# Kernel tuning notes

Measured on AMD Instinct MI355X. Metric: run time of the kernel, lower is better.

The kernel has to match this reference:

```python
import jax, jax.numpy as jnp
import numpy as np

B, S, E, H = 2, 2048, 1024, 16
D = E // H  # head_dim = 64


def setup_inputs() -> dict:
    key = jax.random.key(0)
    ks = jax.random.split(key, 8)
    s = 0.02
    return {
        "queries": jax.random.normal(ks[0], (B, S, E), jnp.float32),
        "keys": jax.random.normal(ks[1], (B, S, E), jnp.float32),
        "values": jax.random.normal(ks[2], (B, S, E), jnp.float32),
        "mask": jnp.ones((B, 1, 1, S), jnp.int32),
        "Wq": jax.random.normal(ks[3], (E, E), jnp.float32) * s,
        "bq": jnp.zeros((E,), jnp.float32),
        "Wk": jax.random.normal(ks[4], (E, E), jnp.float32) * s,
        "bk": jnp.zeros((E,), jnp.float32),
        "Wv": jax.random.normal(ks[5], (E, E), jnp.float32) * s,
        "bv": jnp.zeros((E,), jnp.float32),
        "Wo": jax.random.normal(ks[6], (E, E), jnp.float32) * s,
        "bo": jnp.zeros((E,), jnp.float32),
    }


def reference(queries, keys, values, mask, Wq, bq, Wk, bk, Wv, bv, Wo, bo):
    # NOTE: faithful to source, W_v is applied to the `keys` input; `values` is unused.
    q = queries @ Wq.T + bq            # [B,S,E]
    k = keys @ Wk.T + bk               # [B,S,E]
    v = keys @ Wv.T + bv               # [B,S,E]
    q = q.reshape(B, S, H, D)
    k = k.reshape(B, S, H, D)
    v = v.reshape(B, S, H, D)
    scale = 1.0 / jnp.sqrt(jnp.asarray(D, q.dtype))
    scores = jnp.einsum("nqhd,nkhd->nhqk", q, k)   # [B,H,S,S] full score matrix
    scores = jnp.where(mask == 0, jnp.asarray(-1e20, scores.dtype), scores)
    attn = jax.nn.softmax(scores * scale, axis=-1)
    out = jnp.einsum("nhqk,nkhd->nqhd", attn, v).reshape(B, S, E)
    return out @ Wo.T + bo
```

## Files before the change

kernel.cpp:

```cpp
#include <hip/hip_runtime.h>
#include <hip/hip_bf16.h>
#include <stdint.h>

#define NB 2
#define NS 2048
#define NE 1024
#define NH 16
#define ND 64
#define NT 32

typedef __attribute__((ext_vector_type(4))) float f32x4;
typedef __attribute__((ext_vector_type(16))) float f32x16;
typedef __attribute__((ext_vector_type(8))) short s16x8;
typedef __attribute__((ext_vector_type(4))) unsigned short u16x4;
typedef __attribute__((ext_vector_type(2))) unsigned int uint2v;

__device__ __forceinline__ unsigned short f2bf(float f) {
  union { float f; unsigned int i; } u; u.f = f;
  unsigned int r = u.i + 0x7FFFu + ((u.i >> 16) & 1u);
  return (unsigned short)(r >> 16);
}

__device__ __forceinline__ unsigned cvtpk_bf16(float lo, float hi) {
  unsigned r;
  asm("v_cvt_pk_bf16_f32 %0, %1, %2" : "=v"(r) : "v"(lo), "v"(hi));
  return r;
}

__device__ __forceinline__ void gload_lds16(const void* g, void* l) {
  __builtin_amdgcn_global_load_lds(
      (const __attribute__((address_space(1))) uint32_t*)g,
      (__attribute__((address_space(3))) uint32_t*)l, 16, 0, 0);
}

__device__ __forceinline__ f32x4 mfma16(s16x8 a, s16x8 b, f32x4 c) {
  return __builtin_amdgcn_mfma_f32_16x16x32_bf16(a, b, c, 0, 0, 0);
}
__device__ __forceinline__ f32x16 mfma32(s16x8 a, s16x8 b, f32x16 c) {
  return __builtin_amdgcn_mfma_f32_32x32x16_bf16(a, b, c, 0, 0, 0);
}

__global__ void conv_x2(const float* __restrict__ a, const float* __restrict__ b,
                        unsigned short* __restrict__ da, unsigned short* __restrict__ db,
                        int n4) {
  const float* s = blockIdx.y ? b : a;
  unsigned short* d = blockIdx.y ? db : da;
  int i = blockIdx.x * blockDim.x + threadIdx.x;
  int stride = gridDim.x * blockDim.x;
  for (; i < n4; i += stride) {
    float4 v = ((const float4*)s)[i];
    u16x4 o;
    o.x = f2bf(v.x); o.y = f2bf(v.y); o.z = f2bf(v.z); o.w = f2bf(v.w);
    ((u16x4*)d)[i] = o;
  }
}

__global__ void conv_w4(const float* __restrict__ s0, const float* __restrict__ s1,
                        const float* __restrict__ s2, const float* __restrict__ s3,
                        unsigned short* __restrict__ d0, unsigned short* __restrict__ d1,
                        unsigned short* __restrict__ d2, unsigned short* __restrict__ d3,
                        int n4) {
  const float* s; unsigned short* d;
  switch (blockIdx.y) {
    case 0: s = s0; d = d0; break;
    case 1: s = s1; d = d1; break;
    case 2: s = s2; d = d2; break;
    default: s = s3; d = d3; break;
  }
  int i = blockIdx.x * blockDim.x + threadIdx.x;
  int stride = gridDim.x * blockDim.x;
  for (; i < n4; i += stride) {
    float4 v = ((const float4*)s)[i];
    u16x4 o;
    o.x = f2bf(v.x); o.y = f2bf(v.y); o.z = f2bf(v.z); o.w = f2bf(v.w);
    ((u16x4*)d)[i] = o;
  }
}

__global__ void mask_pack(const int* __restrict__ mask, unsigned long long* __restrict__ bm) {
  int w = blockIdx.x;
  int lane = threadIdx.x;
  int mk = mask[w * 64 + lane];
  unsigned long long bal = __ballot(mk != 0);
  if (lane == 0) bm[w] = bal;
}

__global__ __launch_bounds__(256, 3) void gemm_qkv(
    const unsigned short* __restrict__ Aq, const unsigned short* __restrict__ Akv,
    const unsigned short* __restrict__ Wqp, const unsigned short* __restrict__ Wkp,
    const unsigned short* __restrict__ Wvp,
    const float* __restrict__ bqp, const float* __restrict__ bkp, const float* __restrict__ bvp,
    unsigned short* __restrict__ outq, unsigned short* __restrict__ outk,
    unsigned short* __restrict__ outvt) {
  constexpr int BM = 64, K = 1024;
  __shared__ char smem[2 * (BM * 128 + 16384)];
  const int t = threadIdx.x;
  const int lane = t & 63;
  const int wv = t >> 6;
  const int wr = wv >> 1, wc = wv & 1;
  const int x = blockIdx.x;
  const int bm = blockIdx.y * BM;
  const int lr = lane & 15, lg = lane >> 4;

  const unsigned short* A; const unsigned short* Wp; const float* bp;
  unsigned short* outp; int nloc, mode;
  float qsc;
  if (x < 8)       { A = Aq;  Wp = Wqp; bp = bqp; outp = outq;  nloc = x * 128;        mode = 0; qsc = 0.18033688f; }
  else if (x < 16) { A = Akv; Wp = Wkp; bp = bkp; outp = outk;  nloc = (x - 8) * 128;  mode = 0; qsc = 1.0f; }
  else             { A = Akv; Wp = Wvp; bp = bvp; outp = outvt; nloc = (x - 16) * 128; mode = 1; qsc = 1.0f; }

  f32x4 acc[2][4] = {};

  auto stage = [&](int buf, int k0) {
    char* As = smem + buf * (BM * 128 + 16384);
    char* Bs = As + BM * 128;
#pragma unroll
    for (int r = 0; r < 2; ++r) {
      int lin = r * 256 + t;
      int row = lin >> 3;
      int scb = ((lin & 7) << 4) ^ ((row & 7) << 4);
      gload_lds16((const char*)(A + (size_t)(bm + row) * K + k0) + scb,
                  As + (size_t)(r * 256 + (t & ~63)) * 16);
    }
#pragma unroll
    for (int r = 0; r < 4; ++r) {
      int lin = r * 256 + t;
      int row = lin >> 3;
      int scb = ((lin & 7) << 4) ^ ((row & 7) << 4);
      gload_lds16((const char*)(Wp + (size_t)(nloc + row) * K + k0) + scb,
                  Bs + (size_t)(r * 256 + (t & ~63)) * 16);
    }
  };

  stage(0, 0);
  for (int t6 = 0; t6 < K / 64; ++t6) {
    const int cur = t6 & 1;
    if (t6 + 1 < K / 64) {
      stage(cur ^ 1, (t6 + 1) * 64);
      asm volatile("s_waitcnt vmcnt(6)" ::: "memory");
    } else {
      asm volatile("s_waitcnt vmcnt(0)" ::: "memory");
    }
    asm volatile("s_barrier" ::: "memory");

    const char* As = smem + cur * (BM * 128 + 16384);
    const char* Bs = As + BM * 128;
    s16x8 af[2][2], bfr[4][2];
#pragma unroll
    for (int mf = 0; mf < 2; ++mf)
#pragma unroll
      for (int kk = 0; kk < 2; ++kk) {
        int row = wr * 32 + mf * 16 + lr;
        int cb = (lg << 4) + (kk << 6);
        af[mf][kk] = *(const s16x8*)(As + row * 128 + (cb ^ ((row & 7) << 4)));
      }
#pragma unroll
    for (int nf = 0; nf < 4; ++nf)
#pragma unroll
      for (int kk = 0; kk < 2; ++kk) {
        int row = wc * 64 + nf * 16 + lr;
        int cb = (lg << 4) + (kk << 6);
        bfr[nf][kk] = *(const s16x8*)(Bs + row * 128 + (cb ^ ((row & 7) << 4)));
      }
#pragma unroll
    for (int mf = 0; mf < 2; ++mf)
#pragma unroll
      for (int nf = 0; nf < 4; ++nf)
#pragma unroll
        for (int kk = 0; kk < 2; ++kk)
          acc[mf][nf] = mfma16(af[mf][kk], bfr[nf][kk], acc[mf][nf]);

    asm volatile("s_waitcnt lgkmcnt(0)" ::: "memory");
    asm volatile("s_barrier" ::: "memory");
  }

#pragma unroll
  for (int mf = 0; mf < 2; ++mf)
#pragma unroll
    for (int nf = 0; nf < 4; ++nf) {
      int m0 = bm + wr * 32 + mf * 16 + (lg << 2);
      int nc = wc * 64 + nf * 16 + lr;
      float bv = bp[nloc + nc];
      if (mode == 0) {
#pragma unroll
        for (int r = 0; r < 4; ++r)
          outp[(size_t)(m0 + r) * 1024 + nloc + nc] = f2bf((acc[mf][nf][r] + bv) * qsc);
      } else {
        int b = m0 >> 11, s = m0 & 2047;
        u16x4 o;
        o.x = f2bf(acc[mf][nf][0] + bv);
        o.y = f2bf(acc[mf][nf][1] + bv);
        o.z = f2bf(acc[mf][nf][2] + bv);
        o.w = f2bf(acc[mf][nf][3] + bv);
        *(u16x4*)&outp[((size_t)b * NE + nloc + nc) * NS + s] = o;
      }
    }
}

__global__ __launch_bounds__(256, 3) void gemm_o(
    const unsigned short* __restrict__ A, const unsigned short* __restrict__ W,
    const float* __restrict__ bias, float* __restrict__ out) {
  constexpr int BM = 64, K = 1024;
  __shared__ char smem[2 * (BM * 128 + 16384)];
  const int t = threadIdx.x;
  const int lane = t & 63;
  const int wv = t >> 6;
  const int wr = wv >> 1, wc = wv & 1;
  const int bm = blockIdx.y * BM, bn = blockIdx.x * 128;
  const int lr = lane & 15, lg = lane >> 4;

  f32x4 acc[2][4] = {};

  auto stage = [&](int buf, int k0) {
    char* As = smem + buf * (BM * 128 + 16384);
    char* Bs = As + BM * 128;
#pragma unroll
    for (int r = 0; r < 2; ++r) {
      int lin = r * 256 + t;
      int row = lin >> 3;
      int scb = ((lin & 7) << 4) ^ ((row & 7) << 4);
      gload_lds16((const char*)(A + (size_t)(bm + row) * K + k0) + scb,
                  As + (size_t)(r * 256 + (t & ~63)) * 16);
    }
#pragma unroll
    for (int r = 0; r < 4; ++r) {
      int lin = r * 256 + t;
      int row = lin >> 3;
      int scb = ((lin & 7) << 4) ^ ((row & 7) << 4);
      gload_lds16((const char*)(W + (size_t)(bn + row) * K + k0) + scb,
                  Bs + (size_t)(r * 256 + (t & ~63)) * 16);
    }
  };

  stage(0, 0);
  for (int t6 = 0; t6 < K / 64; ++t6) {
    const int cur = t6 & 1;
    if (t6 + 1 < K / 64) {
      stage(cur ^ 1, (t6 + 1) * 64);
      asm volatile("s_waitcnt vmcnt(6)" ::: "memory");
    } else {
      asm volatile("s_waitcnt vmcnt(0)" ::: "memory");
    }
    asm volatile("s_barrier" ::: "memory");

    const char* As = smem + cur * (BM * 128 + 16384);
    const char* Bs = As + BM * 128;
    s16x8 af[2][2], bfr[4][2];
#pragma unroll
    for (int mf = 0; mf < 2; ++mf)
#pragma unroll
      for (int kk = 0; kk < 2; ++kk) {
        int row = wr * 32 + mf * 16 + lr;
        int cb = (lg << 4) + (kk << 6);
        af[mf][kk] = *(const s16x8*)(As + row * 128 + (cb ^ ((row & 7) << 4)));
      }
#pragma unroll
    for (int nf = 0; nf < 4; ++nf)
#pragma unroll
      for (int kk = 0; kk < 2; ++kk) {
        int row = wc * 64 + nf * 16 + lr;
        int cb = (lg << 4) + (kk << 6);
        bfr[nf][kk] = *(const s16x8*)(Bs + row * 128 + (cb ^ ((row & 7) << 4)));
      }
#pragma unroll
    for (int mf = 0; mf < 2; ++mf)
#pragma unroll
      for (int nf = 0; nf < 4; ++nf)
#pragma unroll
        for (int kk = 0; kk < 2; ++kk)
          acc[mf][nf] = mfma16(af[mf][kk], bfr[nf][kk], acc[mf][nf]);

    asm volatile("s_waitcnt lgkmcnt(0)" ::: "memory");
    asm volatile("s_barrier" ::: "memory");
  }

#pragma unroll
  for (int mf = 0; mf < 2; ++mf)
#pragma unroll
    for (int nf = 0; nf < 4; ++nf) {
      int m0 = bm + wr * 32 + mf * 16 + (lg << 2);
      int n = bn + wc * 64 + nf * 16 + lr;
      float bv = bias[n];
#pragma unroll
      for (int r = 0; r < 4; ++r)
        out[(size_t)(m0 + r) * 1024 + n] = acc[mf][nf][r] + bv;
    }
}

__global__ __launch_bounds__(256, 2) void attn_fwd(
    const unsigned short* __restrict__ qb, const unsigned short* __restrict__ kb,
    const unsigned short* __restrict__ vt, const unsigned long long* __restrict__ bmw,
    unsigned short* __restrict__ ob) {
  __shared__ char smem[65536];
  const int t = threadIdx.x, lane = t & 63, wv = t >> 6;
  const int l31 = lane & 31, hi = lane >> 5;
  const int sw = (l31 & 15) << 4;
  const int bh = blockIdx.y, b = bh >> 4, h = bh & 15;
  const int q = blockIdx.x * 128 + wv * 32 + l31;

  s16x8 qf[4];
#pragma unroll
  for (int ks = 0; ks < 4; ++ks)
    qf[ks] = *(const s16x8*)&qb[((size_t)(b * NS + q)) * NE + h * ND + ks * 16 + hi * 8];

  unsigned long long mword = bmw[(size_t)b * 32 + l31];
  unsigned mlo = (unsigned)mword, mhi = (unsigned)(mword >> 32);

  const char* kSrc[2]; const char* vSrc[2]; int ldsK[2], ldsV[2];
#pragma unroll
  for (int r = 0; r < 2; ++r) {
    int L = (r * 256 + t) * 16;
    int row = L >> 8;
    int offp = (L & 255) ^ ((row & 15) << 4);
    int rr = row + ((offp >> 7) << 5);
    int byo = offp & 127;
    kSrc[r] = (const char*)&kb[((size_t)(b * NS) + rr) * NE + h * ND] + byo;
    vSrc[r] = (const char*)&vt[((size_t)((b * NH + h) * ND) + rr) * NS] + byo;
    ldsK[r] = (r * 256 + (t & ~63)) * 16;
    ldsV[r] = 8192 + ldsK[r];
  }

  int off16[8];
#pragma unroll
  for (int j = 0; j < 8; ++j)
    off16[j] = l31 * 256 + ((j * 32 + hi * 16) ^ sw);

  auto stage = [&](int buf, int kt) {
    char* base = smem + buf * 16384;
#pragma unroll
    for (int r = 0; r < 2; ++r)
      gload_lds16(kSrc[r] + (size_t)kt * (NE * 2), base + ldsK[r]);
#pragma unroll
    for (int r = 0; r < 2; ++r)
      gload_lds16(vSrc[r] + (size_t)kt * 2, base + ldsV[r]);
  };

  f32x16 oacc[2] = {};
  f32x16 lacc = {};
  s16x8 pfp[4];

  auto qk = [&](const char* Ks, f32x16& st0, f32x16& st1) {
#pragma unroll
    for (int ks = 0; ks < 4; ++ks) {
      s16x8 kf = *(const s16x8*)(Ks + off16[ks]);
      st0 = mfma32(kf, qf[ks], st0);
    }
#pragma unroll
    for (int ks = 0; ks < 4; ++ks) {
      s16x8 kf = *(const s16x8*)(Ks + off16[4 + ks]);
      st1 = mfma32(kf, qf[ks], st1);
    }
  };

  auto pv = [&](const char* Vs) {
#pragma unroll
    for (int td = 0; td < 2; ++td)
#pragma unroll
      for (int ks = 0; ks < 4; ++ks) {
        s16x8 vf = *(const s16x8*)(Vs + off16[td * 4 + ks]);
        oacc[td] = mfma32(vf, pfp[ks], oacc[td]);
      }
  };

  auto smpack = [&](int tt, f32x16& st0, f32x16& st1) {
#pragma unroll
    for (int r = 0; r < 16; ++r) st0[r] = __builtin_amdgcn_exp2f(st0[r] - 6.0f);
#pragma unroll
    for (int r = 0; r < 16; ++r) st1[r] = __builtin_amdgcn_exp2f(st1[r] - 6.0f);

    unsigned lo = (unsigned)__builtin_amdgcn_readlane((int)mlo, tt);
    unsigned hh = (unsigned)__builtin_amdgcn_readlane((int)mhi, tt);
    unsigned long long bal = ((unsigned long long)hh << 32) | lo;
    if (bal != ~0ull) {
#pragma unroll
      for (int r = 0; r < 16; ++r) {
        int key0 = (r & 3) + 8 * (r >> 2) + 4 * hi;
        if (!((bal >> key0) & 1)) st0[r] = 0.f;
        if (!((bal >> (key0 + 32)) & 1)) st1[r] = 0.f;
      }
    }

    lacc += st0;
    lacc += st1;

#pragma unroll
    for (int ks = 0; ks < 4; ++ks) {
      const int r0 = (ks & 1) * 8;
      unsigned wreg[4];
#pragma unroll
      for (int w = 0; w < 2; ++w) {
        float e0, e1, e2, e3;
        if (ks < 2) {
          e0 = st0[r0 + 2 * w]; e1 = st0[r0 + 2 * w + 1];
          e2 = st0[r0 + 4 + 2 * w]; e3 = st0[r0 + 4 + 2 * w + 1];
        } else {
          e0 = st1[r0 + 2 * w]; e1 = st1[r0 + 2 * w + 1];
          e2 = st1[r0 + 4 + 2 * w]; e3 = st1[r0 + 4 + 2 * w + 1];
        }
        unsigned x = cvtpk_bf16(e0, e1);
        unsigned y = cvtpk_bf16(e2, e3);
        uint2v r2 = __builtin_amdgcn_permlane32_swap(x, y, false, false);
        wreg[w] = r2.x;
        wreg[w + 2] = r2.y;
      }
      union { unsigned u[4]; s16x8 v; } pu;
      pu.u[0] = wreg[0]; pu.u[1] = wreg[1]; pu.u[2] = wreg[2]; pu.u[3] = wreg[3];
      pfp[ks] = pu.v;
    }
  };

  stage(0, 0);
  stage(1, 64);

  asm volatile("s_waitcnt vmcnt(4)" ::: "memory");
  __builtin_amdgcn_s_barrier();
  stage(2, 128);
  {
    f32x16 s0 = {}, s1 = {};
    __builtin_amdgcn_s_setprio(1);
    qk(smem, s0, s1);
    __builtin_amdgcn_s_setprio(0);
    smpack(0, s0, s1);
  }

#pragma unroll 1
  for (int tt = 1; tt < NT; ++tt) {
    if (tt + 1 < NT) {
      asm volatile("s_waitcnt vmcnt(4)" ::: "memory");
    } else {
      asm volatile("s_waitcnt vmcnt(0)" ::: "memory");
    }
    __builtin_amdgcn_s_barrier();
    if (tt + 2 < NT) stage((tt + 2) & 3, (tt + 2) * 64);

    const char* Kb = smem + (tt & 3) * 16384;
    const char* Vb = smem + ((tt - 1) & 3) * 16384 + 8192;
    f32x16 s0 = {}, s1 = {};
    __builtin_amdgcn_s_setprio(1);
    qk(Kb, s0, s1);
    pv(Vb);
    __builtin_amdgcn_s_setprio(0);
    smpack(tt, s0, s1);
  }

  __builtin_amdgcn_s_setprio(1);
  pv(smem + ((NT - 1) & 3) * 16384 + 8192);
  __builtin_amdgcn_s_setprio(0);

  float l0 = 0.f;
#pragma unroll
  for (int r = 0; r < 16; ++r) l0 += lacc[r];
  float l = l0 + __shfl_xor(l0, 32);
  float inv = 1.0f / l;

  char* Ob = smem + wv * 4096;
#pragma unroll
  for (int td = 0; td < 2; ++td)
#pragma unroll
    for (int i = 0; i < 8; ++i) {
      int r = 2 * i;
      int d = td * 32 + (r & 3) + 8 * (r >> 2) + 4 * hi;
      unsigned pk = cvtpk_bf16(oacc[td][r] * inv, oacc[td][r + 1] * inv);
      *(unsigned*)(Ob + l31 * 128 + ((d * 2) ^ ((l31 & 7) << 4))) = pk;
    }
#pragma unroll
  for (int p4 = 0; p4 < 4; ++p4) {
    int lq = p4 * 8 + (lane >> 3);
    int col = (lane & 7) * 16;
    s16x8 v0 = *(const s16x8*)(Ob + lq * 128 + (col ^ ((lq & 7) << 4)));
    int qg = blockIdx.x * 128 + wv * 32 + lq;
    *(s16x8*)((char*)&ob[((size_t)(b * NS + qg)) * NE + h * ND] + col) = v0;
  }
}

extern "C" void kernel_launch(void* const* d_in, const int* in_sizes, int n_in,
                              void* d_out, int out_size, void* d_ws, size_t ws_size,
                              hipStream_t stream) {
  const float* queries = (const float*)d_in[0];
  const float* keys = (const float*)d_in[1];
  const int* mask = (const int*)d_in[3];
  const float* Wq = (const float*)d_in[4];
  const float* bq = (const float*)d_in[5];
  const float* Wk = (const float*)d_in[6];
  const float* bk = (const float*)d_in[7];
  const float* Wv = (const float*)d_in[8];
  const float* bv = (const float*)d_in[9];
  const float* Wo = (const float*)d_in[10];
  const float* bo = (const float*)d_in[11];
  float* out = (float*)d_out;

  char* ws = (char*)d_ws;
  const size_t SZ_X = (size_t)NB * NS * NE * 2;
  const size_t SZ_W = (size_t)NE * NE * 2;
  unsigned short* qbf = (unsigned short*)(ws);
  unsigned short* kbf = (unsigned short*)(ws + SZ_X);
  unsigned short* wqb = (unsigned short*)(ws + 2 * SZ_X);
  unsigned short* wkb = (unsigned short*)(ws + 2 * SZ_X + SZ_W);
  unsigned short* wvb = (unsigned short*)(ws + 2 * SZ_X + 2 * SZ_W);
  unsigned short* wob = (unsigned short*)(ws + 2 * SZ_X + 3 * SZ_W);
  unsigned short* qp  = (unsigned short*)(ws + 2 * SZ_X + 4 * SZ_W);
  unsigned short* kp  = (unsigned short*)(ws + 3 * SZ_X + 4 * SZ_W);
  unsigned short* vtp = (unsigned short*)(ws + 4 * SZ_X + 4 * SZ_W);
  unsigned short* ao  = (unsigned short*)(ws + 5 * SZ_X + 4 * SZ_W);
  unsigned long long* bmp = (unsigned long long*)(ws + 6 * SZ_X + 4 * SZ_W);

  int nX4 = NB * NS * NE / 4, nW4 = NE * NE / 4;
  conv_x2<<<dim3(1024, 2), 256, 0, stream>>>(queries, keys, qbf, kbf, nX4);
  conv_w4<<<dim3(256, 4), 256, 0, stream>>>(Wq, Wk, Wv, Wo, wqb, wkb, wvb, wob, nW4);
  mask_pack<<<NB * NS / 64, 64, 0, stream>>>(mask, bmp);

  gemm_qkv<<<dim3(24, 64), 256, 0, stream>>>(qbf, kbf, wqb, wkb, wvb,
                                             bq, bk, bv, qp, kp, vtp);

  dim3 ga(NS / 128, NB * NH);
  attn_fwd<<<ga, 256, 0, stream>>>(qp, kp, vtp, bmp, ao);

  gemm_o<<<dim3(8, 64), 256, 0, stream>>>(ao, wob, bo, out);
}
```

Baseline: 115.7 us.

## Split attention over key halves with combine pass; enlarge QKV GEMM tile

The attention kernel now splits the key sequence into two halves along a new grid dimension. Each half writes an unnormalized partial output and a row-sum partial. A new combine kernel adds the two and normalizes. This doubles the attention block count, and with a smaller LDS footprint and a pipeline of 2 K buffers and 3 V buffers it allows more blocks per CU. The QKV GEMM tile grows from 64 to 128 rows to improve operand reuse, at the cost of lower occupancy. The risks are an extra kernel launch, the round trip of the partial outputs through memory, and the partials being rounded to bf16 before they are summed. The split skips the running-max rescale, which is safe only because the code subtracts a fixed offset inside exp2.

```diff
diff --git a/kernel.cpp b/kernel.cpp
--- a/kernel.cpp
+++ b/kernel.cpp
@@ -7,7 +7,7 @@
 #define NE 1024
 #define NH 16
 #define ND 64
-#define NT 32
+#define NTS 16
 
 typedef __attribute__((ext_vector_type(4))) float f32x4;
 typedef __attribute__((ext_vector_type(16))) float f32x16;
@@ -19,6 +19,9 @@
   union { float f; unsigned int i; } u; u.f = f;
   unsigned int r = u.i + 0x7FFFu + ((u.i >> 16) & 1u);
   return (unsigned short)(r >> 16);
+}
+__device__ __forceinline__ float bf2f(unsigned short u) {
+  union { unsigned int i; float f; } x; x.i = ((unsigned int)u) << 16; return x.f;
 }
 
 __device__ __forceinline__ unsigned cvtpk_bf16(float lo, float hi) {
@@ -85,37 +88,38 @@
   if (lane == 0) bm[w] = bal;
 }
 
-__global__ __launch_bounds__(256, 3) void gemm_qkv(
+__global__ __launch_bounds__(256, 2) void gemm_qkv(
     const unsigned short* __restrict__ Aq, const unsigned short* __restrict__ Akv,
     const unsigned short* __restrict__ Wqp, const unsigned short* __restrict__ Wkp,
     const unsigned short* __restrict__ Wvp,
     const float* __restrict__ bqp, const float* __restrict__ bkp, const float* __restrict__ bvp,
     unsigned short* __restrict__ outq, unsigned short* __restrict__ outk,
     unsigned short* __restrict__ outvt) {
-  constexpr int BM = 64, K = 1024;
-  __shared__ char smem[2 * (BM * 128 + 16384)];
+  constexpr int K = 1024;
+  __shared__ char smem[65536];
   const int t = threadIdx.x;
   const int lane = t & 63;
   const int wv = t >> 6;
   const int wr = wv >> 1, wc = wv & 1;
   const int x = blockIdx.x;
-  const int bm = blockIdx.y * BM;
+  const int bm = blockIdx.y * 128;
   const int lr = lane & 15, lg = lane >> 4;
 
   const unsigned short* A; const unsigned short* Wp; const float* bp;
-  unsigned short* outp; int nloc, mode;
+  unsigned short* outp; int mode;
   float qsc;
-  if (x < 8)       { A = Aq;  Wp = Wqp; bp = bqp; outp = outq;  nloc = x * 128;        mode = 0; qsc = 0.18033688f; }
-  else if (x < 16) { A = Akv; Wp = Wkp; bp = bkp; outp = outk;  nloc = (x - 8) * 128;  mode = 0; qsc = 1.0f; }
-  else             { A = Akv; Wp = Wvp; bp = bvp; outp = outvt; nloc = (x - 16) * 128; mode = 1; qsc = 1.0f; }
-
-  f32x4 acc[2][4] = {};
+  const int nloc = (x & 7) * 128;
+  if (x < 8)       { A = Aq;  Wp = Wqp; bp = bqp; outp = outq;  mode = 0; qsc = 0.18033688f; }
+  else if (x < 16) { A = Akv; Wp = Wkp; bp = bkp; outp = outk;  mode = 0; qsc = 1.0f; }
+  else             { A = Akv; Wp = Wvp; bp = bvp; outp = outvt; mode = 1; qsc = 1.0f; }
+
+  f32x4 acc[4][4] = {};
 
   auto stage = [&](int buf, int k0) {
-    char* As = smem + buf * (BM * 128 + 16384);
-    char* Bs = As + BM * 128;
-#pragma unroll
-    for (int r = 0; r < 2; ++r) {
+    char* As = smem + buf * 32768;
+    char* Bs = As + 16384;
+#pragma unroll
+    for (int r = 0; r < 4; ++r) {
       int lin = r * 256 + t;
       int row = lin >> 3;
       int scb = ((lin & 7) << 4) ^ ((row & 7) << 4);
@@ -137,20 +141,20 @@
     const int cur = t6 & 1;
     if (t6 + 1 < K / 64) {
       stage(cur ^ 1, (t6 + 1) * 64);
-      asm volatile("s_waitcnt vmcnt(6)" ::: "memory");
+      asm volatile("s_waitcnt vmcnt(8)" ::: "memory");
     } else {
       asm volatile("s_waitcnt vmcnt(0)" ::: "memory");
     }
     asm volatile("s_barrier" ::: "memory");
 
-    const char* As = smem + cur * (BM * 128 + 16384);
-    const char* Bs = As + BM * 128;
-    s16x8 af[2][2], bfr[4][2];
-#pragma unroll
-    for (int mf = 0; mf < 2; ++mf)
+    const char* As = smem + cur * 32768;
+    const char* Bs = As + 16384;
+    s16x8 af[4][2], bfr[4][2];
+#pragma unroll
+    for (int mf = 0; mf < 4; ++mf)
 #pragma unroll
       for (int kk = 0; kk < 2; ++kk) {
-        int row = wr * 32 + mf * 16 + lr;
+        int row = wr * 64 + mf * 16 + lr;
         int cb = (lg << 4) + (kk << 6);
         af[mf][kk] = *(const s16x8*)(As + row * 128 + (cb ^ ((row & 7) << 4)));
       }
@@ -163,7 +167,7 @@
         bfr[nf][kk] = *(const s16x8*)(Bs + row * 128 + (cb ^ ((row & 7) << 4)));
       }
 #pragma unroll
-    for (int mf = 0; mf < 2; ++mf)
+    for (int mf = 0; mf < 4; ++mf)
 #pragma unroll
       for (int nf = 0; nf < 4; ++nf)
 #pragma unroll
@@ -175,10 +179,10 @@
   }
 
 #pragma unroll
-  for (int mf = 0; mf < 2; ++mf)
+  for (int mf = 0; mf < 4; ++mf)
 #pragma unroll
     for (int nf = 0; nf < 4; ++nf) {
-      int m0 = bm + wr * 32 + mf * 16 + (lg << 2);
+      int m0 = bm + wr * 64 + mf * 16 + (lg << 2);
       int nc = wc * 64 + nf * 16 + lr;
       float bv = bp[nloc + nc];
       if (mode == 0) {
@@ -287,16 +291,20 @@
     }
 }
 
-__global__ __launch_bounds__(256, 2) void attn_fwd(
+__global__ __launch_bounds__(256, 4) void attn_fwd(
     const unsigned short* __restrict__ qb, const unsigned short* __restrict__ kb,
     const unsigned short* __restrict__ vt, const unsigned long long* __restrict__ bmw,
-    unsigned short* __restrict__ ob) {
-  __shared__ char smem[65536];
+    unsigned short* __restrict__ op0, unsigned short* __restrict__ op1,
+    float* __restrict__ lp) {
+  __shared__ char smem[40960];
   const int t = threadIdx.x, lane = t & 63, wv = t >> 6;
   const int l31 = lane & 31, hi = lane >> 5;
   const int sw = (l31 & 15) << 4;
   const int bh = blockIdx.y, b = bh >> 4, h = bh & 15;
+  const int sp = blockIdx.z;
+  const int kbase = sp * 1024;
   const int q = blockIdx.x * 128 + wv * 32 + l31;
+  unsigned short* opp = sp ? op1 : op0;
 
   s16x8 qf[4];
 #pragma unroll
@@ -306,7 +314,7 @@
   unsigned long long mword = bmw[(size_t)b * 32 + l31];
   unsigned mlo = (unsigned)mword, mhi = (unsigned)(mword >> 32);
 
-  const char* kSrc[2]; const char* vSrc[2]; int ldsK[2], ldsV[2];
+  const char* kSrc[2]; const char* vSrc[2]; int ldsO[2];
 #pragma unroll
   for (int r = 0; r < 2; ++r) {
     int L = (r * 256 + t) * 16;
@@ -314,10 +322,9 @@
     int offp = (L & 255) ^ ((row & 15) << 4);
     int rr = row + ((offp >> 7) << 5);
     int byo = offp & 127;
-    kSrc[r] = (const char*)&kb[((size_t)(b * NS) + rr) * NE + h * ND] + byo;
-    vSrc[r] = (const char*)&vt[((size_t)((b * NH + h) * ND) + rr) * NS] + byo;
-    ldsK[r] = (r * 256 + (t & ~63)) * 16;
-    ldsV[r] = 8192 + ldsK[r];
+    kSrc[r] = (const char*)&kb[((size_t)(b * NS + kbase) + rr) * NE + h * ND] + byo;
+    vSrc[r] = (const char*)&vt[((size_t)((b * NH + h) * ND) + rr) * NS + kbase] + byo;
+    ldsO[r] = (r * 256 + (t & ~63)) * 16;
   }
 
   int off16[8];
@@ -325,14 +332,15 @@
   for (int j = 0; j < 8; ++j)
     off16[j] = l31 * 256 + ((j * 32 + hi * 16) ^ sw);
 
-  auto stage = [&](int buf, int kt) {
-    char* base = smem + buf * 16384;
+  auto stage = [&](int j) {
+    char* kb_ = smem + (j & 1) * 8192;
+    char* vb_ = smem + 16384 + (j % 3) * 8192;
 #pragma unroll
     for (int r = 0; r < 2; ++r)
-      gload_lds16(kSrc[r] + (size_t)kt * (NE * 2), base + ldsK[r]);
+      gload_lds16(kSrc[r] + (size_t)j * (64 * NE * 2), kb_ + ldsO[r]);
 #pragma unroll
     for (int r = 0; r < 2; ++r)
-      gload_lds16(vSrc[r] + (size_t)kt * 2, base + ldsV[r]);
+      gload_lds16(vSrc[r] + (size_t)j * (64 * 2), vb_ + ldsO[r]);
   };
 
   f32x16 oacc[2] = {};
@@ -368,8 +376,9 @@
 #pragma unroll
     for (int r = 0; r < 16; ++r) st1[r] = __builtin_amdgcn_exp2f(st1[r] - 6.0f);
 
-    unsigned lo = (unsigned)__builtin_amdgcn_readlane((int)mlo, tt);
-    unsigned hh = (unsigned)__builtin_amdgcn_readlane((int)mhi, tt);
+    int g = sp * NTS + tt;
+    unsigned lo = (unsigned)__builtin_amdgcn_readlane((int)mlo, g);
+    unsigned hh = (unsigned)__builtin_amdgcn_readlane((int)mhi, g);
     unsigned long long bal = ((unsigned long long)hh << 32) | lo;
     if (bal != ~0ull) {
 #pragma unroll
@@ -409,12 +418,10 @@
     }
   };
 
-  stage(0, 0);
-  stage(1, 64);
-
-  asm volatile("s_waitcnt vmcnt(4)" ::: "memory");
+  stage(0);
+  asm volatile("s_waitcnt vmcnt(0)" ::: "memory");
   __builtin_amdgcn_s_barrier();
-  stage(2, 128);
+  stage(1);
   {
     f32x16 s0 = {}, s1 = {};
     __builtin_amdgcn_s_setprio(1);
@@ -424,17 +431,13 @@
   }
 
 #pragma unroll 1
-  for (int tt = 1; tt < NT; ++tt) {
-    if (tt + 1 < NT) {
-      asm volatile("s_waitcnt vmcnt(4)" ::: "memory");
-    } else {
-      asm volatile("s_waitcnt vmcnt(0)" ::: "memory");
-    }
+  for (int tt = 1; tt < NTS; ++tt) {
+    asm volatile("s_waitcnt vmcnt(0)" ::: "memory");
     __builtin_amdgcn_s_barrier();
-    if (tt + 2 < NT) stage((tt + 2) & 3, (tt + 2) * 64);
-
-    const char* Kb = smem + (tt & 3) * 16384;
-    const char* Vb = smem + ((tt - 1) & 3) * 16384 + 8192;
+    if (tt + 1 < NTS) stage(tt + 1);
+
+    const char* Kb = smem + (tt & 1) * 8192;
+    const char* Vb = smem + 16384 + ((tt - 1) % 3) * 8192;
     f32x16 s0 = {}, s1 = {};
     __builtin_amdgcn_s_setprio(1);
     qk(Kb, s0, s1);
@@ -444,15 +447,16 @@
   }
 
   __builtin_amdgcn_s_setprio(1);
-  pv(smem + ((NT - 1) & 3) * 16384 + 8192);
+  pv(smem + 16384 + ((NTS - 1) % 3) * 8192);
   __builtin_amdgcn_s_setprio(0);
 
   float l0 = 0.f;
 #pragma unroll
   for (int r = 0; r < 16; ++r) l0 += lacc[r];
   float l = l0 + __shfl_xor(l0, 32);
-  float inv = 1.0f / l;
-
+  if (hi == 0) lp[(((size_t)sp * NB + b) * NH + h) * NS + q] = l;
+
+  __syncthreads();
   char* Ob = smem + wv * 4096;
 #pragma unroll
   for (int td = 0; td < 2; ++td)
@@ -460,7 +464,7 @@
     for (int i = 0; i < 8; ++i) {
       int r = 2 * i;
       int d = td * 32 + (r & 3) + 8 * (r >> 2) + 4 * hi;
-      unsigned pk = cvtpk_bf16(oacc[td][r] * inv, oacc[td][r + 1] * inv);
+      unsigned pk = cvtpk_bf16(oacc[td][r], oacc[td][r + 1]);
       *(unsigned*)(Ob + l31 * 128 + ((d * 2) ^ ((l31 & 7) << 4))) = pk;
     }
 #pragma unroll
@@ -469,8 +473,37 @@
     int col = (lane & 7) * 16;
     s16x8 v0 = *(const s16x8*)(Ob + lq * 128 + (col ^ ((lq & 7) << 4)));
     int qg = blockIdx.x * 128 + wv * 32 + lq;
-    *(s16x8*)((char*)&ob[((size_t)(b * NS + qg)) * NE + h * ND] + col) = v0;
-  }
+    *(s16x8*)((char*)&opp[((size_t)(b * NS + qg)) * NE + h * ND] + col) = v0;
+  }
+}
+
+__global__ void attn_combine(const unsigned short* __restrict__ o0,
+                             const unsigned short* __restrict__ o1,
+                             const float* __restrict__ lp,
+                             unsigned short* __restrict__ ao) {
+  int idx = blockIdx.x * 256 + threadIdx.x;
+  size_t f = (size_t)idx * 8;
+  int b = (int)(f >> 21);
+  int s = (int)((f >> 10) & 2047);
+  int h = (int)((f >> 6) & 15);
+  float l0 = lp[((size_t)(b * NH + h)) * NS + s];
+  float l1 = lp[(size_t)NB * NH * NS + ((size_t)(b * NH + h)) * NS + s];
+  float inv = 1.0f / (l0 + l1);
+  s16x8 a0 = ((const s16x8*)o0)[idx];
+  s16x8 a1 = ((const s16x8*)o1)[idx];
+  u16x4 r0, r1;
+#pragma unroll
+  for (int j = 0; j < 4; ++j) {
+    float v = (bf2f((unsigned short)a0[j]) + bf2f((unsigned short)a1[j])) * inv;
+    ((unsigned short*)&r0)[j] = f2bf(v);
+  }
+#pragma unroll
+  for (int j = 0; j < 4; ++j) {
+    float v = (bf2f((unsigned short)a0[4 + j]) + bf2f((unsigned short)a1[4 + j])) * inv;
+    ((unsigned short*)&r1)[j] = f2bf(v);
+  }
+  ((u16x4*)ao)[idx * 2] = r0;
+  ((u16x4*)ao)[idx * 2 + 1] = r1;
 }
 
 extern "C" void kernel_launch(void* const* d_in, const int* in_sizes, int n_in,
@@ -503,17 +536,21 @@
   unsigned short* vtp = (unsigned short*)(ws + 4 * SZ_X + 4 * SZ_W);
   unsigned short* ao  = (unsigned short*)(ws + 5 * SZ_X + 4 * SZ_W);
   unsigned long long* bmp = (unsigned long long*)(ws + 6 * SZ_X + 4 * SZ_W);
+  unsigned short* op0 = qbf;
+  unsigned short* op1 = kbf;
+  float* lpart = (float*)wqb;
 
   int nX4 = NB * NS * NE / 4, nW4 = NE * NE / 4;
   conv_x2<<<dim3(1024, 2), 256, 0, stream>>>(queries, keys, qbf, kbf, nX4);
   conv_w4<<<dim3(256, 4), 256, 0, stream>>>(Wq, Wk, Wv, Wo, wqb, wkb, wvb, wob, nW4);
   mask_pack<<<NB * NS / 64, 64, 0, stream>>>(mask, bmp);
 
-  gemm_qkv<<<dim3(24, 64), 256, 0, stream>>>(qbf, kbf, wqb, wkb, wvb,
+  gemm_qkv<<<dim3(24, 32), 256, 0, stream>>>(qbf, kbf, wqb, wkb, wvb,
                                              bq, bk, bv, qp, kp, vtp);
 
-  dim3 ga(NS / 128, NB * NH);
-  attn_fwd<<<ga, 256, 0, stream>>>(qp, kp, vtp, bmp, ao);
+  dim3 ga(NS / 128, NB * NH, 2);
+  attn_fwd<<<ga, 256, 0, stream>>>(qp, kp, vtp, bmp, op0, op1, lpart);
+  attn_combine<<<4096, 256, 0, stream>>>(op0, op1, lpart, ao);
 
   gemm_o<<<dim3(8, 64), 256, 0, stream>>>(ao, wob, bo, out);
 }
```

Measured after the change: 162.9 us. 1.41x slower.
